# Optimization experiments

Measured on AMD Instinct MI355X. Metric: run time of the kernel, lower is better.

## Reference

```python
import jax, jax.numpy as jnp
import numpy as np

EPS = 1e-05  # matches tf entropy epsilon


def setup_inputs() -> dict:
    key = jax.random.key(0)
    k1, k2 = jax.random.split(key)
    encodings = jax.random.normal(k1, (8192, 64), dtype=jnp.float32)
    categorical = jax.random.uniform(k2, (8192, 25), dtype=jnp.float32)
    return {"encodings": encodings, "categorical": categorical, "k": 15}


def reference(encodings, categorical, k):
    B = encodings.shape[0]
    n_components = categorical.shape[1]
    k = min(k, B // 4)  # layer clamps k to batch_size // 4

    hard_groups = jnp.argmax(categorical, axis=1)           # [B] int
    max_groups = jnp.max(categorical, axis=1)               # [B]

    # Batched brute-force kNN. tf.norm's sqrt is monotonic, so the strict
    # comparison `dist < kth_dist` is identical on squared distances; working
    # in squared space avoids sqrt(0) issues and an extra pass.
    sq = jnp.sum(encodings * encodings, axis=1)             # [B]
    d2 = sq[:, None] + sq[None, :] - 2.0 * (encodings @ encodings.T)
    d2 = jnp.maximum(d2, 0.0)                               # [B, B]

    # (k+1)-smallest distances per row (0-indexed k, self-distance included,
    # matching tf.gather(tf.sort(distances), k)).
    neg_topk, _ = jax.lax.top_k(-d2, k + 1)                 # [B, k+1]
    kth = -neg_topk[:, k]                                   # [B] k-th smallest

    mask = (d2 < kth[:, None]).astype(jnp.float32)          # [B, B] strict <

    # Per-row label histogram over the neighborhood: counts[i,c] = #neighbors
    # of i in cluster c. Zero bins contribute 0 to -sum(b*log(b+eps)), same as
    # tf.bincount's variable-length output.
    onehot = jax.nn.one_hot(hard_groups, n_components, dtype=jnp.float32)
    counts = mask @ onehot                                  # [B, n_components]
    n_i = jnp.sum(counts, axis=-1, keepdims=True)           # [B, 1]
    bins = counts / jnp.maximum(n_i, 1.0)
    neighbourhood_entropy = -jnp.sum(bins * jnp.log(bins + EPS), axis=-1)  # [B]

    # Global cluster-size entropy + number of populated clusters.
    gcounts = jnp.sum(onehot, axis=0)                       # [n_components]
    gbins = gcounts / jnp.float32(B)
    cluster_size_entropy = -jnp.sum(gbins * jnp.log(gbins + EPS))
    n_populated = jnp.sum(gcounts > 0).astype(jnp.float32)

    return encodings, neighbourhood_entropy, cluster_size_entropy, n_populated, max_groups
```

## Files before the change

### kernel.cpp

```cpp
#include <hip/hip_runtime.h>
#include <math.h>

#define Bsz    8192
#define Dd     64
#define NC     25
#define RT     16
#define TILES  64
#define KCAP   16
#define EPSf   1e-5f

typedef short  short8  __attribute__((ext_vector_type(8)));
typedef float  floatx4 __attribute__((ext_vector_type(4)));


__device__ inline unsigned short f2bf(float x) {
    unsigned u = __float_as_uint(x);
    u += 0x7FFFu + ((u >> 16) & 1u);
    return (unsigned short)(u >> 16);
}
__device__ inline float bf2f(unsigned short h) { return __uint_as_float(((unsigned)h) << 16); }

__device__ inline void bsort16(unsigned* a) {
    #pragma unroll
    for (int k = 2; k <= 16; k <<= 1)
        #pragma unroll
        for (int j = k >> 1; j > 0; j >>= 1)
            #pragma unroll
            for (int i = 0; i < 16; ++i) {
                int l = i ^ j;
                if (l > i) {
                    bool up = ((i & k) == 0) || (k == 16);
                    unsigned x = a[i], y = a[l];
                    unsigned lo = (x < y) ? x : y, hi = (x < y) ? y : x;
                    a[i] = up ? lo : hi;
                    a[l] = up ? hi : lo;
                }
            }
}
__device__ inline void bclean16(unsigned* t) {
    #pragma unroll
    for (int j = 8; j > 0; j >>= 1)
        #pragma unroll
        for (int i = 0; i < 16; ++i) {
            int l = i ^ j;
            if (l > i) {
                unsigned x = t[i], y = t[l];
                t[i] = (x < y) ? x : y;
                t[l] = (x < y) ? y : x;
            }
        }
}
__device__ inline void bmerge16(unsigned* ls, const unsigned* b) {
    unsigned t[16];
    #pragma unroll
    for (int i = 0; i < 16; ++i) { unsigned x = ls[i], y = b[15 - i]; t[i] = (x < y) ? x : y; }
    bclean16(t);
    #pragma unroll
    for (int i = 0; i < 16; ++i) ls[i] = t[i];
}
__device__ inline void bmerge16_shfl(unsigned* ls, int mask) {
    unsigned t[16];
    #pragma unroll
    for (int i = 0; i < 16; ++i) {
        unsigned pv = (unsigned)__shfl_xor((int)ls[15 - i], mask);
        unsigned x = ls[i];
        t[i] = (x < pv) ? x : pv;
    }
    bclean16(t);
    #pragma unroll
    for (int i = 0; i < 16; ++i) ls[i] = t[i];
}

__device__ inline void compute_pair(
    short8 ah0, short8 ah1, short8 al0, short8 al1,
    short8 ch0, short8 ch1, short8 cl0, short8 cl1,
    uint4 sva, uint4 svb,
    const short8* bh, const short8* bl, float sqi,
    unsigned* cand, int off)
{
    floatx4 accA = (floatx4){0.f, 0.f, 0.f, 0.f};
    floatx4 accB = (floatx4){0.f, 0.f, 0.f, 0.f};
    accA = __builtin_amdgcn_mfma_f32_16x16x32_bf16(ah0, bh[0], accA, 0, 0, 0);
    accB = __builtin_amdgcn_mfma_f32_16x16x32_bf16(ch0, bh[0], accB, 0, 0, 0);
    accA = __builtin_amdgcn_mfma_f32_16x16x32_bf16(ah0, bl[0], accA, 0, 0, 0);
    accB = __builtin_amdgcn_mfma_f32_16x16x32_bf16(ch0, bl[0], accB, 0, 0, 0);
    accA = __builtin_amdgcn_mfma_f32_16x16x32_bf16(al0, bh[0], accA, 0, 0, 0);
    accB = __builtin_amdgcn_mfma_f32_16x16x32_bf16(cl0, bh[0], accB, 0, 0, 0);
    accA = __builtin_amdgcn_mfma_f32_16x16x32_bf16(ah1, bh[1], accA, 0, 0, 0);
    accB = __builtin_amdgcn_mfma_f32_16x16x32_bf16(ch1, bh[1], accB, 0, 0, 0);
    accA = __builtin_amdgcn_mfma_f32_16x16x32_bf16(ah1, bl[1], accA, 0, 0, 0);
    accB = __builtin_amdgcn_mfma_f32_16x16x32_bf16(ch1, bl[1], accB, 0, 0, 0);
    accA = __builtin_amdgcn_mfma_f32_16x16x32_bf16(al1, bh[1], accA, 0, 0, 0);
    accB = __builtin_amdgcn_mfma_f32_16x16x32_bf16(cl1, bh[1], accB, 0, 0, 0);

    unsigned sa[4] = {sva.x, sva.y, sva.z, sva.w};
    unsigned sb[4] = {svb.x, svb.y, svb.z, svb.w};
    #pragma unroll
    for (int r = 0; r < 4; ++r) {
        float d2a = fmaxf(sqi + __uint_as_float(sa[r] & ~31u) + accA[r], 0.f);
        cand[off + r]     = (__float_as_uint(d2a) & ~31u) | (sa[r] & 31u);
        float d2b = fmaxf(sqi + __uint_as_float(sb[r] & ~31u) + accB[r], 0.f);
        cand[off + 4 + r] = (__float_as_uint(d2b) & ~31u) | (sb[r] & 31u);
    }
}


__global__ __launch_bounds__(256) void pre_kernel(
    const float* __restrict__ enc, const float* __restrict__ cat,
    unsigned int* __restrict__ slab,
    char* __restrict__ enc1, char* __restrict__ enc2,
    float* __restrict__ out_max, float* __restrict__ out_enc)
{
    const int gid = blockIdx.x * 256 + threadIdx.x;
    const int p = gid >> 5, pr = gid & 31;

    float2 ev = ((const float2*)enc)[gid];
    ((float2*)out_enc)[gid] = ev;

    float s = ev.x * ev.x + ev.y * ev.y;
    #pragma unroll
    for (int m = 1; m < 32; m <<= 1) s += __shfl_xor(s, m, 32);

    {
        const int g = p >> 4, c15p = p & 15;
        const int d0 = 2 * pr, kh = d0 >> 5, q = (d0 >> 3) & 3, e0 = d0 & 7;
        const int base = g * 4096 + kh * 1024 + (q * 16 + c15p) * 16 + e0 * 2;
        unsigned short ha = f2bf(ev.x), hb = f2bf(ev.y);
        unsigned short la = f2bf(ev.x - bf2f(ha)), lb = f2bf(ev.y - bf2f(hb));
        *(unsigned*)(enc1 + base)        = (unsigned)ha | ((unsigned)hb << 16);
        *(unsigned*)(enc1 + base + 2048) = (unsigned)la | ((unsigned)lb << 16);
        float y0 = -2.f * ev.x, y1 = -2.f * ev.y;
        unsigned short hc = f2bf(y0), hd = f2bf(y1);
        unsigned short lc = f2bf(y0 - bf2f(hc)), ld = f2bf(y1 - bf2f(hd));
        *(unsigned*)(enc2 + base)        = (unsigned)hc | ((unsigned)hd << 16);
        *(unsigned*)(enc2 + base + 2048) = (unsigned)lc | ((unsigned)ld << 16);
    }
    float cv = (pr < NC) ? cat[p * NC + pr] : -1.f;
    int ci = pr;
    #pragma unroll
    for (int m = 1; m < 32; m <<= 1) {
        float ov = __shfl_xor(cv, m, 32);
        int   oi = __shfl_xor(ci, m, 32);
        if (ov > cv || (ov == cv && oi < ci)) { cv = ov; ci = oi; }
    }
    if (pr == 0) {
        out_max[p] = cv;
        slab[p] = (__float_as_uint(s) & ~31u) | (unsigned)ci;
    }
}

__global__ __launch_bounds__(512, 4) void main_kernel(
    const char* __restrict__ enc1, const char* __restrict__ enc2,
    const unsigned int* __restrict__ slab, const int* __restrict__ kptr,
    float* __restrict__ out_ent, float* __restrict__ out_glob)
{
    __shared__ unsigned wl[8 * 16 * 17];
    __shared__ int cnt[32];

    const int tid  = threadIdx.x, bid = blockIdx.x;
    const int wv   = tid >> 6, lane = tid & 63;
    const int quad = (tid >> 4) & 3, c15 = tid & 15;
    const int rowbase = bid * RT;

    short8 bh[2], bl[2];
    {
        const char* ib = enc1 + (size_t)bid * 4096 + lane * 16;
        bh[0] = *(const short8*)(ib);
        bh[1] = *(const short8*)(ib + 1024);
        bl[0] = *(const short8*)(ib + 2048);
        bl[1] = *(const short8*)(ib + 3072);
    }
    const float sqi = __uint_as_float(slab[rowbase + c15] & ~31u);

    unsigned ls[KCAP];
    #pragma unroll
    for (int q = 0; q < KCAP; ++q) ls[q] = 0xFFFFFFFFu;
    unsigned cand[16];

    const char* jp = enc2 + (size_t)wv * 4096 + lane * 16;
    const unsigned* sp = slab + wv * 16 + quad * 4;

    short8 Ah0 = *(const short8*)(jp);
    short8 Ah1 = *(const short8*)(jp + 1024);
    short8 Al0 = *(const short8*)(jp + 2048);
    short8 Al1 = *(const short8*)(jp + 3072);
    short8 Ch0 = *(const short8*)(jp + 32768);
    short8 Ch1 = *(const short8*)(jp + 33792);
    short8 Cl0 = *(const short8*)(jp + 34816);
    short8 Cl1 = *(const short8*)(jp + 35840);
    uint4  Asva = *(const uint4*)(sp);
    uint4  Asvb = *(const uint4*)(sp + 128);

    for (int t = 0; t < TILES; t += 4) {
        jp += 65536; sp += 256;
        short8 Bh0 = *(const short8*)(jp);
        short8 Bh1 = *(const short8*)(jp + 1024);
        short8 Bl0 = *(const short8*)(jp + 2048);
        short8 Bl1 = *(const short8*)(jp + 3072);
        short8 Dh0 = *(const short8*)(jp + 32768);
        short8 Dh1 = *(const short8*)(jp + 33792);
        short8 Dl0 = *(const short8*)(jp + 34816);
        short8 Dl1 = *(const short8*)(jp + 35840);
        uint4  Bsva = *(const uint4*)(sp);
        uint4  Bsvb = *(const uint4*)(sp + 128);
        compute_pair(Ah0, Ah1, Al0, Al1, Ch0, Ch1, Cl0, Cl1, Asva, Asvb,
                     bh, bl, sqi, cand, 0);
        jp += 65536; sp += 256;
        Ah0 = *(const short8*)(jp);
        Ah1 = *(const short8*)(jp + 1024);
        Al0 = *(const short8*)(jp + 2048);
        Al1 = *(const short8*)(jp + 3072);
        Ch0 = *(const short8*)(jp + 32768);
        Ch1 = *(const short8*)(jp + 33792);
        Cl0 = *(const short8*)(jp + 34816);
        Cl1 = *(const short8*)(jp + 35840);
        Asva = *(const uint4*)(sp);
        Asvb = *(const uint4*)(sp + 128);
        compute_pair(Bh0, Bh1, Bl0, Bl1, Dh0, Dh1, Dl0, Dl1, Bsva, Bsvb,
                     bh, bl, sqi, cand, 8);
        bsort16(cand);
        bmerge16(ls, cand);
    }

    if (bid == 0) {
        if (tid < 32) cnt[tid] = 0;
        __syncthreads();
        for (int i = tid; i < Bsz; i += 512) atomicAdd(&cnt[slab[i] & 31u], 1);
        __syncthreads();
        if (tid == 0) {
            float gent = 0.f, npop = 0.f;
            for (int i = 0; i < NC; ++i) {
                int g = cnt[i];
                if (g > 0) {
                    npop += 1.f;
                    float gb = (float)g / (float)Bsz;
                    gent -= gb * logf(gb + EPSf);
                }
            }
            out_glob[0] = gent;
            out_glob[1] = npop;
        }
        __syncthreads();
    }

    bmerge16_shfl(ls, 16);
    bmerge16_shfl(ls, 32);
    if (quad == 0) {
        #pragma unroll
        for (int q = 0; q < KCAP; ++q) wl[(wv * 16 + c15) * 17 + q] = ls[q];
    }
    __syncthreads();
    if (wv == 0) {
        const int row = tid >> 2, sub = tid & 3;
        unsigned A[16], Bv[16];
        #pragma unroll
        for (int i = 0; i < 16; ++i) A[i]  = wl[((2 * sub)     * 16 + row) * 17 + i];
        #pragma unroll
        for (int i = 0; i < 16; ++i) Bv[i] = wl[((2 * sub + 1) * 16 + row) * 17 + i];
        bmerge16(A, Bv);
        bmerge16_shfl(A, 1);
        bmerge16_shfl(A, 2);

        int kk = kptr[0];
        if (kk > Bsz / 4) kk = Bsz / 4;
        if (kk > KCAP - 1) kk = KCAP - 1;

        unsigned kth = A[15];
        #pragma unroll
        for (int q = 0; q < 16; ++q) if (q == kk) kth = A[q];
        int nn = 0;
        #pragma unroll
        for (int t = 0; t < 15; ++t) nn += (t < kk && A[t] < kth) ? 1 : 0;

        float inv = 1.f / (float)((nn > 0) ? nn : 1);
        float part = 0.f;
        #pragma unroll
        for (int a4 = 0; a4 < 4; ++a4) {
            int a = sub + 4 * a4;
            if (a < nn) {
                int la = (int)(A[a] & 31u);
                int c = 0;
                #pragma unroll
                for (int b = 0; b < 15; ++b) c += (b < nn && (int)(A[b] & 31u) == la) ? 1 : 0;
                part -= inv * logf((float)c * inv + EPSf);
            }
        }
        part += __shfl_xor(part, 1);
        part += __shfl_xor(part, 2);
        if (sub == 0) out_ent[rowbase + row] = part;
    }
}

extern "C" void kernel_launch(void* const* d_in, const int* in_sizes, int n_in,
                              void* d_out, int out_size, void* d_ws, size_t ws_size,
                              hipStream_t stream)
{
    const float* enc  = (const float*)d_in[0];
    const float* cat  = (const float*)d_in[1];
    const int*   kptr = (const int*)d_in[2];
    float* out = (float*)d_out;

    unsigned int* slab = (unsigned int*)d_ws;
    char*         enc1 = (char*)d_ws + 32768;
    char*         enc2 = (char*)d_ws + 2129920;

    float* out_enc  = out;
    float* out_ent  = out + Bsz * Dd;
    float* out_glob = out + Bsz * Dd + Bsz;
    float* out_max  = out + Bsz * Dd + Bsz + 2;

    pre_kernel<<<1024, 256, 0, stream>>>(enc, cat, slab, enc1, enc2, out_max, out_enc);
    main_kernel<<<Bsz / RT, 512, 0, stream>>>(enc1, enc2, slab, kptr, out_ent, out_glob);
}
```

Baseline: 124.1 us.

## Split each row tile across 16 waves with staggered column starts and odd-even sort

Each block now runs 16 waves instead of 8, so every wave scans half as many column tiles. The start offset is wrapped with a mask, which staggers where waves begin reading the column data. The final cross-wave merge now folds four partial lists per sub-lane instead of two. The bitonic candidate sort is swapped for a Batcher odd-even merge sort, which uses fewer compare-exchanges. In exchange, the larger block needs more registers per CU, and the launch bounds of (1024, 8) may force register spilling.

Result: slower. 135.4 us (+9.1%).

```diff
diff --git a/kernel.cpp b/kernel.cpp
--- a/kernel.cpp
+++ b/kernel.cpp
@@ -5,9 +5,10 @@
 #define Dd     64
 #define NC     25
 #define RT     16
-#define TILES  64
+#define WAVES  16
 #define KCAP   16
 #define EPSf   1e-5f
+#define JMASK  2097151u
 
 typedef short  short8  __attribute__((ext_vector_type(8)));
 typedef float  floatx4 __attribute__((ext_vector_type(4)));
@@ -20,22 +21,25 @@
 }
 __device__ inline float bf2f(unsigned short h) { return __uint_as_float(((unsigned)h) << 16); }
 
-__device__ inline void bsort16(unsigned* a) {
-    #pragma unroll
-    for (int k = 2; k <= 16; k <<= 1)
-        #pragma unroll
-        for (int j = k >> 1; j > 0; j >>= 1)
+__device__ inline void oesort16(unsigned* a) {
+    #pragma unroll
+    for (int p = 1; p < 16; p <<= 1) {
+        #pragma unroll
+        for (int k = p; k >= 1; k >>= 1) {
             #pragma unroll
-            for (int i = 0; i < 16; ++i) {
-                int l = i ^ j;
-                if (l > i) {
-                    bool up = ((i & k) == 0) || (k == 16);
-                    unsigned x = a[i], y = a[l];
-                    unsigned lo = (x < y) ? x : y, hi = (x < y) ? y : x;
-                    a[i] = up ? lo : hi;
-                    a[l] = up ? hi : lo;
+            for (int j = (k & (p - 1)); j + k < 16; j += 2 * k) {
+                #pragma unroll
+                for (int i = 0; i < k; ++i) {
+                    if (i + j + k < 16 &&
+                        ((i + j) / (2 * p)) == ((i + j + k) / (2 * p))) {
+                        unsigned x = a[i + j], y = a[i + j + k];
+                        a[i + j]     = (x < y) ? x : y;
+                        a[i + j + k] = (x < y) ? y : x;
+                    }
                 }
             }
+        }
+    }
 }
 __device__ inline void bclean16(unsigned* t) {
     #pragma unroll
@@ -149,12 +153,12 @@
     }
 }
 
-__global__ __launch_bounds__(512, 4) void main_kernel(
+__global__ __launch_bounds__(1024, 8) void main_kernel(
     const char* __restrict__ enc1, const char* __restrict__ enc2,
     const unsigned int* __restrict__ slab, const int* __restrict__ kptr,
     float* __restrict__ out_ent, float* __restrict__ out_glob)
 {
-    __shared__ unsigned wl[8 * 16 * 17];
+    __shared__ unsigned wl[WAVES * 16 * 17];
     __shared__ int cnt[32];
 
     const int tid  = threadIdx.x, bid = blockIdx.x;
@@ -177,55 +181,56 @@
     for (int q = 0; q < KCAP; ++q) ls[q] = 0xFFFFFFFFu;
     unsigned cand[16];
 
-    const char* jp = enc2 + (size_t)wv * 4096 + lane * 16;
+    const char* jb = enc2 + lane * 16;
+    unsigned jo = (unsigned)wv * 4096u;
     const unsigned* sp = slab + wv * 16 + quad * 4;
 
-    short8 Ah0 = *(const short8*)(jp);
-    short8 Ah1 = *(const short8*)(jp + 1024);
-    short8 Al0 = *(const short8*)(jp + 2048);
-    short8 Al1 = *(const short8*)(jp + 3072);
-    short8 Ch0 = *(const short8*)(jp + 32768);
-    short8 Ch1 = *(const short8*)(jp + 33792);
-    short8 Cl0 = *(const short8*)(jp + 34816);
-    short8 Cl1 = *(const short8*)(jp + 35840);
+    short8 Ah0 = *(const short8*)(jb + jo);
+    short8 Ah1 = *(const short8*)(jb + jo + 1024);
+    short8 Al0 = *(const short8*)(jb + jo + 2048);
+    short8 Al1 = *(const short8*)(jb + jo + 3072);
+    short8 Ch0 = *(const short8*)(jb + jo + 65536);
+    short8 Ch1 = *(const short8*)(jb + jo + 66560);
+    short8 Cl0 = *(const short8*)(jb + jo + 67584);
+    short8 Cl1 = *(const short8*)(jb + jo + 68608);
     uint4  Asva = *(const uint4*)(sp);
-    uint4  Asvb = *(const uint4*)(sp + 128);
-
-    for (int t = 0; t < TILES; t += 4) {
-        jp += 65536; sp += 256;
-        short8 Bh0 = *(const short8*)(jp);
-        short8 Bh1 = *(const short8*)(jp + 1024);
-        short8 Bl0 = *(const short8*)(jp + 2048);
-        short8 Bl1 = *(const short8*)(jp + 3072);
-        short8 Dh0 = *(const short8*)(jp + 32768);
-        short8 Dh1 = *(const short8*)(jp + 33792);
-        short8 Dl0 = *(const short8*)(jp + 34816);
-        short8 Dl1 = *(const short8*)(jp + 35840);
+    uint4  Asvb = *(const uint4*)(sp + 256);
+
+    for (int t = 0; t < 8; ++t) {
+        jo = (jo + 131072u) & JMASK; sp += 512;
+        short8 Bh0 = *(const short8*)(jb + jo);
+        short8 Bh1 = *(const short8*)(jb + jo + 1024);
+        short8 Bl0 = *(const short8*)(jb + jo + 2048);
+        short8 Bl1 = *(const short8*)(jb + jo + 3072);
+        short8 Dh0 = *(const short8*)(jb + jo + 65536);
+        short8 Dh1 = *(const short8*)(jb + jo + 66560);
+        short8 Dl0 = *(const short8*)(jb + jo + 67584);
+        short8 Dl1 = *(const short8*)(jb + jo + 68608);
         uint4  Bsva = *(const uint4*)(sp);
-        uint4  Bsvb = *(const uint4*)(sp + 128);
+        uint4  Bsvb = *(const uint4*)(sp + 256);
         compute_pair(Ah0, Ah1, Al0, Al1, Ch0, Ch1, Cl0, Cl1, Asva, Asvb,
                      bh, bl, sqi, cand, 0);
-        jp += 65536; sp += 256;
-        Ah0 = *(const short8*)(jp);
-        Ah1 = *(const short8*)(jp + 1024);
-        Al0 = *(const short8*)(jp + 2048);
-        Al1 = *(const short8*)(jp + 3072);
-        Ch0 = *(const short8*)(jp + 32768);
-        Ch1 = *(const short8*)(jp + 33792);
-        Cl0 = *(const short8*)(jp + 34816);
-        Cl1 = *(const short8*)(jp + 35840);
+        jo = (jo + 131072u) & JMASK; sp += 512;
+        Ah0 = *(const short8*)(jb + jo);
+        Ah1 = *(const short8*)(jb + jo + 1024);
+        Al0 = *(const short8*)(jb + jo + 2048);
+        Al1 = *(const short8*)(jb + jo + 3072);
+        Ch0 = *(const short8*)(jb + jo + 65536);
+        Ch1 = *(const short8*)(jb + jo + 66560);
+        Cl0 = *(const short8*)(jb + jo + 67584);
+        Cl1 = *(const short8*)(jb + jo + 68608);
         Asva = *(const uint4*)(sp);
-        Asvb = *(const uint4*)(sp + 128);
+        Asvb = *(const uint4*)(sp + 256);
         compute_pair(Bh0, Bh1, Bl0, Bl1, Dh0, Dh1, Dl0, Dl1, Bsva, Bsvb,
                      bh, bl, sqi, cand, 8);
-        bsort16(cand);
+        oesort16(cand);
         bmerge16(ls, cand);
     }
 
     if (bid == 0) {
         if (tid < 32) cnt[tid] = 0;
         __syncthreads();
-        for (int i = tid; i < Bsz; i += 512) atomicAdd(&cnt[slab[i] & 31u], 1);
+        for (int i = tid; i < Bsz; i += 1024) atomicAdd(&cnt[slab[i] & 31u], 1);
         __syncthreads();
         if (tid == 0) {
             float gent = 0.f, npop = 0.f;
@@ -254,9 +259,15 @@
         const int row = tid >> 2, sub = tid & 3;
         unsigned A[16], Bv[16];
         #pragma unroll
-        for (int i = 0; i < 16; ++i) A[i]  = wl[((2 * sub)     * 16 + row) * 17 + i];
-        #pragma unroll
-        for (int i = 0; i < 16; ++i) Bv[i] = wl[((2 * sub + 1) * 16 + row) * 17 + i];
+        for (int i = 0; i < 16; ++i) A[i]  = wl[((4 * sub)     * 16 + row) * 17 + i];
+        #pragma unroll
+        for (int i = 0; i < 16; ++i) Bv[i] = wl[((4 * sub + 1) * 16 + row) * 17 + i];
+        bmerge16(A, Bv);
+        #pragma unroll
+        for (int i = 0; i < 16; ++i) Bv[i] = wl[((4 * sub + 2) * 16 + row) * 17 + i];
+        bmerge16(A, Bv);
+        #pragma unroll
+        for (int i = 0; i < 16; ++i) Bv[i] = wl[((4 * sub + 3) * 16 + row) * 17 + i];
         bmerge16(A, Bv);
         bmerge16_shfl(A, 1);
         bmerge16_shfl(A, 2);
@@ -310,5 +321,5 @@
     float* out_max  = out + Bsz * Dd + Bsz + 2;
 
     pre_kernel<<<1024, 256, 0, stream>>>(enc, cat, slab, enc1, enc2, out_max, out_enc);
-    main_kernel<<<Bsz / RT, 512, 0, stream>>>(enc1, enc2, slab, kptr, out_ent, out_glob);
-}
+    main_kernel<<<Bsz / RT, 1024, 0, stream>>>(enc1, enc2, slab, kptr, out_ent, out_glob);
+}
```
